# Performance work log

Measured on AMD Instinct MI355X. Metric: run time of the kernel, lower is better.

## Reference

```python
import jax, jax.numpy as jnp
import numpy as np

B, L, N, C = 64, 12, 4096, 3
FD, HD, OUT = 32, 64, 12
TID, DIW, TD = 288, 7, 16
STEPS = 4
EMB = 10  # node embedding dim for learned adjacency


def setup_inputs() -> dict:
    key = jax.random.key(0)
    ks = jax.random.split(key, 16)
    g = lambda i, shape, s=0.05: jax.random.normal(ks[i], shape, dtype=jnp.float32) * s
    z = lambda n: jnp.zeros((n,), jnp.float32)
    return {
        "history_data": jax.random.uniform(ks[0], (B, L, N, C), dtype=jnp.float32),
        "future_data": jnp.zeros((B, L, N, 1), jnp.float32),
        "batch_seen": 0,
        "epoch": 0,
        "train": 1,
        "tid_emb": g(1, (TID, TD)),
        "diw_emb": g(2, (DIW, TD)),
        "t2f_w": g(3, (2 * TD, FD)), "t2f_b": z(FD),
        "enc_w1": g(4, (L * C, HD)), "enc_b1": z(HD),
        "enc_w2": g(5, (HD, FD)), "enc_b2": z(FD),
        "node_emb": g(6, (N, EMB), 1.0),
        "pde_w1": g(7, (FD, HD)), "pde_b1": z(HD),
        "pde_w2": g(8, (HD, FD)), "pde_b2": z(FD),
        "ss_win": g(9, (FD, FD)), "ss_wst": g(10, (FD, FD)), "ss_b": z(FD),
        "ss_wout": g(11, (FD, FD)), "ss_bout": z(FD),
        "dec_w1": g(12, (FD, HD)), "dec_b1": z(HD),
        "dec_w2": g(13, (HD, OUT)), "dec_b2": z(OUT),
        "pde_mix": jnp.array(0.5, jnp.float32),
    }


def reference(history_data, future_data, batch_seen, epoch, train,
              tid_emb, diw_emb, t2f_w, t2f_b,
              enc_w1, enc_b1, enc_w2, enc_b2,
              node_emb,
              pde_w1, pde_b1, pde_w2, pde_b2,
              ss_win, ss_wst, ss_b, ss_wout, ss_bout,
              dec_w1, dec_b1, dec_w2, dec_b2, pde_mix):
    # --- encoder: per-node MLP over flattened (L, C) history ---
    x = history_data[..., :C]                                    # [B,L,N,C]
    x = jnp.transpose(x, (0, 2, 1, 3)).reshape(B, N, L * C)      # [B,N,L*C]
    field = jnp.maximum(x @ enc_w1 + enc_b1, 0.0) @ enc_w2 + enc_b2  # [B,N,FD]

    # --- temporal field bias from last-step tid/diw ---
    tid_idx = jnp.clip((history_data[:, -1, :, 1] * TID).astype(jnp.int32), 0, TID - 1)
    diw_idx = jnp.clip((history_data[:, -1, :, 2] * DIW).astype(jnp.int32), 0, DIW - 1)
    temp = jnp.concatenate([tid_emb[tid_idx], diw_emb[diw_idx]], axis=-1)  # [B,N,2*TD]
    field = field + temp @ t2f_w + t2f_b

    # --- learned adjacency for graph Laplacian (L = I - A) ---
    A = jax.nn.softmax(jnp.maximum(node_emb @ node_emb.T, 0.0), axis=-1)  # [N,N]

    alpha = jax.nn.sigmoid(pde_mix)
    dt = 1.0 / STEPS
    state = jnp.zeros_like(field)
    for _ in range(STEPS):  # fixed small unroll over PDE steps
        L_F = jnp.einsum('nm,bmf->bnf', A, field) - field         # (A - I) F
        N_F = jnp.maximum(field @ pde_w1 + pde_b1, 0.0) @ pde_w2 + pde_b2
        fe = field + (alpha * L_F + (1.0 - alpha) * N_F) * dt
        state = jnp.tanh(fe @ ss_win + state @ ss_wst + ss_b)     # state-space update
        field = fe + state @ ss_wout + ss_bout

    # --- decoder: per-node MLP to output horizon ---
    pred = jnp.maximum(field @ dec_w1 + dec_b1, 0.0) @ dec_w2 + dec_b2  # [B,N,OUT]
    return jnp.transpose(pred, (0, 2, 1))[..., None]              # [B,OUT,N,1]
```

## Files before the change

kernel.cpp:

```cpp
#include <hip/hip_runtime.h>

#define BATCH 64
#define LHIST 12
#define NNODE 4096
#define CCH   3
#define FD    32
#define HD    64
#define OUTD  12
#define TIDN  288
#define DIWN  7
#define TDD   16
#define EMBD  10
#define MROWS 2048
#define KDIM  4096
#define MTOT  (BATCH * NNODE)

typedef __attribute__((ext_vector_type(8))) short bf16x8;
typedef __attribute__((ext_vector_type(4))) float f32x4;

union BF8U { bf16x8 v; unsigned short s[8]; };

__device__ __forceinline__ unsigned short f2b(float f) {
    union { float f; unsigned u; } v; v.f = f;
    unsigned r = v.u + 0x7fffu + ((v.u >> 16) & 1u);
    return (unsigned short)(r >> 16);
}

__device__ __forceinline__ float b2f(unsigned short u) {
    union { unsigned u; float f; } v; v.u = (unsigned)u << 16; return v.f;
}

__device__ __forceinline__ float fast_tanh(float x) {
    x = fminf(fmaxf(x, -15.f), 15.f);
    const float e = __expf(2.f * x);
    return (e - 1.f) / (e + 1.f);
}

__device__ __forceinline__ void gl2lds16(const void* g, void* l) {
    __builtin_amdgcn_global_load_lds((__attribute__((address_space(1))) void*)(void*)g,
                                     (__attribute__((address_space(3))) void*)l, 16, 0, 0);
}

__device__ __forceinline__ bf16x8 ldsfrag(const unsigned short* p) {
    return *(const bf16x8*)p;
}

__device__ __forceinline__ bf16x8 pack8(float4 a, float4 b) {
    BF8U u;
    u.s[0] = f2b(a.x); u.s[1] = f2b(a.y); u.s[2] = f2b(a.z); u.s[3] = f2b(a.w);
    u.s[4] = f2b(b.x); u.s[5] = f2b(b.y); u.s[6] = f2b(b.z); u.s[7] = f2b(b.w);
    return u.v;
}

__global__ __launch_bounds__(256) void build_A(const float* __restrict__ emb,
                                               unsigned short* __restrict__ A) {
    const int n = blockIdx.x;
    const int tid = threadIdx.x;
    __shared__ float sc[NNODE];
    __shared__ float red[256];
    float e[EMBD];
#pragma unroll
    for (int c = 0; c < EMBD; c++) e[c] = emb[(size_t)n * EMBD + c];
    float mx = 0.f;
    for (int m = tid; m < NNODE; m += 256) {
        float s = 0.f;
#pragma unroll
        for (int c = 0; c < EMBD; c++) s += e[c] * emb[(size_t)m * EMBD + c];
        s = fmaxf(s, 0.f);
        sc[m] = s;
        mx = fmaxf(mx, s);
    }
    red[tid] = mx;
    __syncthreads();
    for (int off = 128; off > 0; off >>= 1) {
        if (tid < off) red[tid] = fmaxf(red[tid], red[tid + off]);
        __syncthreads();
    }
    mx = red[0];
    __syncthreads();
    float sum = 0.f;
    for (int m = tid; m < NNODE; m += 256) {
        float v = expf(sc[m] - mx);
        sc[m] = v;
        sum += v;
    }
    red[tid] = sum;
    __syncthreads();
    for (int off = 128; off > 0; off >>= 1) {
        if (tid < off) red[tid] += red[tid + off];
        __syncthreads();
    }
    const float inv = 1.f / red[0];
    for (int m = tid; m < NNODE; m += 256)
        A[(size_t)n * NNODE + m] = f2b(sc[m] * inv);
}

__global__ __launch_bounds__(256, 2) void encoder(const float* __restrict__ hist,
                                                  const float* __restrict__ tid_emb,
                                                  const float* __restrict__ diw_emb,
                                                  const float* __restrict__ t2f_w,
                                                  const float* __restrict__ t2f_b,
                                                  const float* __restrict__ enc_w1,
                                                  const float* __restrict__ enc_b1,
                                                  const float* __restrict__ enc_w2,
                                                  const float* __restrict__ enc_b2,
                                                  float* __restrict__ field,
                                                  unsigned short* __restrict__ fT) {
    const int gid = blockIdx.x * 256 + threadIdx.x;
    const int b = gid >> 12;
    const int n = gid & (NNODE - 1);
    const float* hb = hist + ((size_t)b * LHIST * NNODE + n) * CCH;
    float x[LHIST * CCH];
#pragma unroll
    for (int l = 0; l < LHIST; l++) {
        x[l * 3 + 0] = hb[(size_t)l * NNODE * CCH + 0];
        x[l * 3 + 1] = hb[(size_t)l * NNODE * CCH + 1];
        x[l * 3 + 2] = hb[(size_t)l * NNODE * CCH + 2];
    }
    float f[FD];
#pragma unroll
    for (int o = 0; o < FD; o++) f[o] = enc_b2[o] + t2f_b[o];
    for (int j = 0; j < HD; j++) {
        float h = enc_b1[j];
#pragma unroll
        for (int k = 0; k < LHIST * CCH; k++) h += x[k] * enc_w1[k * HD + j];
        h = fmaxf(h, 0.f);
#pragma unroll
        for (int o = 0; o < FD; o++) f[o] += h * enc_w2[j * FD + o];
    }
    const int ti = min(max((int)(x[11 * 3 + 1] * 288.0f), 0), TIDN - 1);
    const int di = min(max((int)(x[11 * 3 + 2] * 7.0f), 0), DIWN - 1);
    for (int g = 0; g < TDD; g++) {
        const float tg = tid_emb[ti * TDD + g];
        const float dg = diw_emb[di * TDD + g];
#pragma unroll
        for (int o = 0; o < FD; o++)
            f[o] += tg * t2f_w[g * FD + o] + dg * t2f_w[(TDD + g) * FD + o];
    }
#pragma unroll
    for (int o4 = 0; o4 < FD / 4; o4++) {
        float4 v = {f[o4 * 4 + 0], f[o4 * 4 + 1], f[o4 * 4 + 2], f[o4 * 4 + 3]};
        *(float4*)&field[(size_t)gid * FD + o4 * 4] = v;
    }
#pragma unroll
    for (int o = 0; o < FD; o++)
        fT[(size_t)(b * FD + o) * NNODE + n] = f2b(f[o]);
}

#define TPAD 36
#define QHP  72
#define QFP  40
__global__ __launch_bounds__(256) void gemm_step(const unsigned short* __restrict__ X,
                                                 const unsigned short* __restrict__ Y,
                                                 float* __restrict__ field,
                                                 unsigned short* __restrict__ state,
                                                 unsigned short* __restrict__ fTo,
                                                 const float* __restrict__ pde_w1,
                                                 const float* __restrict__ pde_b1,
                                                 const float* __restrict__ pde_w2,
                                                 const float* __restrict__ pde_b2,
                                                 const float* __restrict__ ss_win,
                                                 const float* __restrict__ ss_wst,
                                                 const float* __restrict__ ss_b,
                                                 const float* __restrict__ ss_wout,
                                                 const float* __restrict__ ss_bout,
                                                 const float* __restrict__ pde_mix,
                                                 int first) {
    constexpr int K = KDIM;
    constexpr int BK = 32;
    __shared__ __align__(16) unsigned short SM0[512 * TPAD];
    __shared__ __align__(16) unsigned short W1T[HD * FD];
    __shared__ __align__(16) unsigned short W2T[FD * HD];
    __shared__ __align__(16) unsigned short WinT[FD * FD];
    __shared__ __align__(16) unsigned short WstT[FD * FD];
    __shared__ __align__(16) unsigned short WoutT[FD * FD];
    __shared__ __align__(16) unsigned short Hs[4 * 32 * QHP];
    __shared__ __align__(16) unsigned short Fs[4 * 32 * QFP];

    const int tid = threadIdx.x;
    const int wave = tid >> 6;
    const int lane = tid & 63;

    for (int i = tid; i < HD * FD; i += 256) W1T[(i & 63) * FD + (i >> 6)] = f2b(pde_w1[i]);
    for (int i = tid; i < HD * FD; i += 256) W2T[(i & 31) * HD + (i >> 5)] = f2b(pde_w2[i]);
    for (int i = tid; i < FD * FD; i += 256) {
        WinT [(i & 31) * FD + (i >> 5)] = f2b(ss_win[i]);
        WstT [(i & 31) * FD + (i >> 5)] = f2b(ss_wst[i]);
        WoutT[(i & 31) * FD + (i >> 5)] = f2b(ss_wout[i]);
    }

    const int l = blockIdx.x + 16 * blockIdx.y;
    const int xcd = l & 7;
    const int rem = l >> 3;
    const int by = xcd * 4 + (rem & 3);
    const int bx = rem >> 2;
    const int i0 = bx * 128;
    const int j0 = by * 128;
    const int b0 = i0 >> 5;

    const int wi = (wave >> 1) * 64;
    const int wj = (wave & 1) * 64;

    const int lrow = lane >> 2;
    const int gcol = ((lane & 3) ^ ((lane >> 3) & 3)) * 8;

    const unsigned short* Xg = X + (size_t)(i0 + wave * 32 + lrow) * K + gcol;
    const unsigned short* Yg = Y + (size_t)(j0 + wave * 32 + lrow) * K + gcol;
    unsigned short* XsB = SM0;
    unsigned short* YsB = SM0 + 8192;
    unsigned short* Xd0 = XsB + (wave * 32) * BK;
    unsigned short* Xd1 = XsB + (wave * 32 + 16) * BK;
    unsigned short* Yd0 = YsB + (wave * 32) * BK;
    unsigned short* Yd1 = YsB + (wave * 32 + 16) * BK;

    const f32x4 zero = {0.f, 0.f, 0.f, 0.f};
    f32x4 acc[4][4];
#pragma unroll
    for (int a = 0; a < 4; a++)
#pragma unroll
        for (int b = 0; b < 4; b++) acc[a][b] = zero;

    const int fr = lane & 15;
    const int q = lane >> 4;
    const int kq8 = (q ^ ((fr >> 1) & 3)) * 8;

#define GS_ISSUE(P, KT)                                        \
    gl2lds16(Xg + (KT), Xd0 + (P) * 4096);                     \
    gl2lds16(Xg + (KT) + 16 * K, Xd1 + (P) * 4096);            \
    gl2lds16(Yg + (KT), Yd0 + (P) * 4096);                     \
    gl2lds16(Yg + (KT) + 16 * K, Yd1 + (P) * 4096);

#define GS_COMPUTE(P)                                                                 \
    {                                                                                 \
        bf16x8 fa[4], fb[4];                                                          \
        _Pragma("unroll") for (int t = 0; t < 4; t++)                                 \
            fa[t] = *(const bf16x8*)&XsB[(P) * 4096 + (wi + t * 16 + fr) * BK + kq8]; \
        _Pragma("unroll") for (int t = 0; t < 4; t++)                                 \
            fb[t] = *(const bf16x8*)&YsB[(P) * 4096 + (wj + t * 16 + fr) * BK + kq8]; \
        _Pragma("unroll") for (int mi = 0; mi < 4; mi++)                              \
            _Pragma("unroll") for (int ni = 0; ni < 4; ni++)                          \
                acc[mi][ni] = __builtin_amdgcn_mfma_f32_16x16x32_bf16(                \
                    fa[mi], fb[ni], acc[mi][ni], 0, 0, 0);                            \
    }

    GS_ISSUE(0, 0);
    __syncthreads();
    int p = 0;
    for (int kt = 0; kt < K; kt += BK) {
        if (kt + BK < K) { GS_ISSUE(p ^ 1, kt + BK); }
        GS_COMPUTE(p);
        __syncthreads();
        p ^= 1;
    }
#undef GS_COMPUTE
#undef GS_ISSUE

    unsigned short* T = SM0;
    const int r0 = q * 4;
#pragma unroll
    for (int mi = 0; mi < 4; mi++) {
#pragma unroll
        for (int ni = 0; ni < 4; ni++) {
            const int R0 = i0 + wi + mi * 16 + r0;
            const int nl = wj + ni * 16 + fr;
            ushort4 pk = {f2b(acc[mi][ni][0]), f2b(acc[mi][ni][1]),
                          f2b(acc[mi][ni][2]), f2b(acc[mi][ni][3])};
            *(ushort4*)&T[((((R0 >> 5) & 3) << 7) + nl) * TPAD + (R0 & 31)] = pk;
        }
    }
    __syncthreads();

    const int ln = fr;
    const int kq = q * 8;
    unsigned short* Hw = &Hs[wave * 32 * QHP];
    unsigned short* Fw = &Fs[wave * 32 * QFP];
    const float alpha = 1.f / (1.f + __expf(-pde_mix[0]));
    const float dt = 0.25f;

    bf16x8 w1f[4], w2f[2][2], winf[2], wstf[2], woutf[2];
#pragma unroll
    for (int nj = 0; nj < 4; nj++) w1f[nj] = ldsfrag(&W1T[(nj * 16 + ln) * FD + kq]);
#pragma unroll
    for (int nf = 0; nf < 2; nf++) {
#pragma unroll
        for (int kk = 0; kk < 2; kk++)
            w2f[nf][kk] = ldsfrag(&W2T[(nf * 16 + ln) * HD + kk * 32 + kq]);
        winf[nf]  = ldsfrag(&WinT [(nf * 16 + ln) * FD + kq]);
        wstf[nf]  = ldsfrag(&WstT [(nf * 16 + ln) * FD + kq]);
        woutf[nf] = ldsfrag(&WoutT[(nf * 16 + ln) * FD + kq]);
    }
    float b1v[4], b2v[2], bsv[2], bov[2];
#pragma unroll
    for (int nj = 0; nj < 4; nj++) b1v[nj] = pde_b1[nj * 16 + ln];
#pragma unroll
    for (int nf = 0; nf < 2; nf++) {
        b2v[nf] = pde_b2[nf * 16 + ln];
        bsv[nf] = ss_b[nf * 16 + ln];
        bov[nf] = ss_bout[nf * 16 + ln];
    }

    for (int qtr = 0; qtr < 4; qtr++) {
        const int lb = wave * 128 + qtr * 32;
        const int bb = lb >> 7;
        const int nl0 = lb & 127;
        const int bg = b0 + bb;
        const int mwg = (bg << 12) + j0 + nl0;

        bf16x8 fA[2], stA[2];
#pragma unroll
        for (int mi = 0; mi < 2; mi++) {
            const float4* fp = (const float4*)&field[(size_t)(mwg + mi * 16 + ln) * FD + kq];
            fA[mi] = pack8(fp[0], fp[1]);
        }
        if (!first) {
#pragma unroll
            for (int mi = 0; mi < 2; mi++)
                stA[mi] = *(const bf16x8*)&state[(size_t)(mwg + mi * 16 + ln) * FD + kq];
        }

        f32x4 hc[2][4];
#pragma unroll
        for (int mi = 0; mi < 2; mi++)
#pragma unroll
            for (int nj = 0; nj < 4; nj++)
                hc[mi][nj] = __builtin_amdgcn_mfma_f32_16x16x32_bf16(fA[mi], w1f[nj], zero, 0, 0, 0);
#pragma unroll
        for (int mi = 0; mi < 2; mi++)
#pragma unroll
            for (int nj = 0; nj < 4; nj++)
#pragma unroll
                for (int r = 0; r < 4; r++)
                    Hw[(mi * 16 + r0 + r) * QHP + nj * 16 + ln] =
                        f2b(fmaxf(hc[mi][nj][r] + b1v[nj], 0.f));

        float fld[2][2][4], ctv[2][2][4];
#pragma unroll
        for (int mi = 0; mi < 2; mi++)
#pragma unroll
            for (int nf = 0; nf < 2; nf++)
#pragma unroll
                for (int r = 0; r < 4; r++) {
                    const size_t idx = (size_t)(mwg + mi * 16 + r0 + r) * FD + nf * 16 + ln;
                    fld[mi][nf][r] = field[idx];
                    ctv[mi][nf][r] = b2f(T[(lb + mi * 16 + r0 + r) * TPAD + nf * 16 + ln]);
                }

        bf16x8 hA[2][2];
#pragma unroll
        for (int mi = 0; mi < 2; mi++)
#pragma unroll
            for (int kk = 0; kk < 2; kk++)
                hA[mi][kk] = ldsfrag(&Hw[(mi * 16 + ln) * QHP + kk * 32 + kq]);
        f32x4 nc[2][2];
#pragma unroll
        for (int mi = 0; mi < 2; mi++)
#pragma unroll
            for (int nf = 0; nf < 2; nf++) {
                f32x4 a = __builtin_amdgcn_mfma_f32_16x16x32_bf16(hA[mi][0], w2f[nf][0], zero, 0, 0, 0);
                nc[mi][nf] = __builtin_amdgcn_mfma_f32_16x16x32_bf16(hA[mi][1], w2f[nf][1], a, 0, 0, 0);
            }

        float fe[2][2][4];
#pragma unroll
        for (int mi = 0; mi < 2; mi++)
#pragma unroll
            for (int nf = 0; nf < 2; nf++)
#pragma unroll
                for (int r = 0; r < 4; r++) {
                    const float nfv = nc[mi][nf][r] + b2v[nf];
                    const float fv = fld[mi][nf][r];
                    fe[mi][nf][r] = fv + (alpha * (ctv[mi][nf][r] - fv) + (1.f - alpha) * nfv) * dt;
                    Fw[(mi * 16 + r0 + r) * QFP + nf * 16 + ln] = f2b(fe[mi][nf][r]);
                }

        bf16x8 feA[2];
#pragma unroll
        for (int mi = 0; mi < 2; mi++) feA[mi] = ldsfrag(&Fw[(mi * 16 + ln) * QFP + kq]);
        f32x4 sc_[2][2];
#pragma unroll
        for (int mi = 0; mi < 2; mi++)
#pragma unroll
            for (int nf = 0; nf < 2; nf++) {
                f32x4 a = __builtin_amdgcn_mfma_f32_16x16x32_bf16(feA[mi], winf[nf], zero, 0, 0, 0);
                if (!first)
                    a = __builtin_amdgcn_mfma_f32_16x16x32_bf16(stA[mi], wstf[nf], a, 0, 0, 0);
                sc_[mi][nf] = a;
            }
        float sval[2][2][4];
#pragma unroll
        for (int mi = 0; mi < 2; mi++)
#pragma unroll
            for (int nf = 0; nf < 2; nf++)
#pragma unroll
                for (int r = 0; r < 4; r++)
                    sval[mi][nf][r] = fast_tanh(sc_[mi][nf][r] + bsv[nf]);
#pragma unroll
        for (int mi = 0; mi < 2; mi++)
#pragma unroll
            for (int nf = 0; nf < 2; nf++)
#pragma unroll
                for (int r = 0; r < 4; r++)
                    Fw[(mi * 16 + r0 + r) * QFP + nf * 16 + ln] = f2b(sval[mi][nf][r]);

        bf16x8 SA[2];
#pragma unroll
        for (int mi = 0; mi < 2; mi++) SA[mi] = ldsfrag(&Fw[(mi * 16 + ln) * QFP + kq]);
#pragma unroll
        for (int mi = 0; mi < 2; mi++) {
#pragma unroll
            for (int nf = 0; nf < 2; nf++) {
                f32x4 oc = __builtin_amdgcn_mfma_f32_16x16x32_bf16(SA[mi], woutf[nf], zero, 0, 0, 0);
                float fnew[4];
#pragma unroll
                for (int r = 0; r < 4; r++) {
                    fnew[r] = fe[mi][nf][r] + oc[r] + bov[nf];
                    const size_t idx = (size_t)(mwg + mi * 16 + r0 + r) * FD + nf * 16 + ln;
                    field[idx] = fnew[r];
                    state[idx] = f2b(sval[mi][nf][r]);
                }
                ushort4 pk = {f2b(fnew[0]), f2b(fnew[1]), f2b(fnew[2]), f2b(fnew[3])};
                const size_t fta = (size_t)(bg * FD + nf * 16 + ln) * NNODE
                                 + j0 + nl0 + mi * 16 + r0;
                *(ushort4*)&fTo[fta] = pk;
            }
        }
    }
}

__global__ __launch_bounds__(256) void gemm_bt(const unsigned short* __restrict__ X,
                                               const unsigned short* __restrict__ Y,
                                               unsigned short* __restrict__ Cp) {
    constexpr int K = KDIM;
    constexpr int KS = KDIM / 2;
    constexpr int BK = 32;
    __shared__ __align__(16) unsigned short Xs[2 * 4096];
    __shared__ __align__(16) unsigned short Ys[2 * 4096];
    const int tid = threadIdx.x;
    const int wave = tid >> 6;
    const int lane = tid & 63;

    const int l = blockIdx.x + 16 * blockIdx.y;
    const int xcd = l & 7;
    const int rem = l >> 3;
    const int by = xcd * 4 + (rem & 3);
    const int bx = rem >> 2;
    const int i0 = bx * 128;
    const int j0 = by * 128;
    const int k0 = blockIdx.z * KS;
    unsigned short* C = Cp + (size_t)blockIdx.z * MTOT * FD;

    const int wi = (wave >> 1) * 64;
    const int wj = (wave & 1) * 64;

    const int lrow = lane >> 2;
    const int gcol = ((lane & 3) ^ ((lane >> 3) & 3)) * 8;

    const unsigned short* Xg = X + (size_t)(i0 + wave * 32 + lrow) * K + k0 + gcol;
    const unsigned short* Yg = Y + (size_t)(j0 + wave * 32 + lrow) * K + k0 + gcol;
    unsigned short* Xd0 = Xs + (wave * 32) * BK;
    unsigned short* Xd1 = Xs + (wave * 32 + 16) * BK;
    unsigned short* Yd0 = Ys + (wave * 32) * BK;
    unsigned short* Yd1 = Ys + (wave * 32 + 16) * BK;

    const f32x4 zero = {0.f, 0.f, 0.f, 0.f};
    f32x4 acc[4][4];
#pragma unroll
    for (int a = 0; a < 4; a++)
#pragma unroll
        for (int b = 0; b < 4; b++) acc[a][b] = zero;

    const int fr = lane & 15;
    const int q = lane >> 4;
    const int kq8 = (q ^ ((fr >> 1) & 3)) * 8;

#define GB_ISSUE(P, KT)                                        \
    gl2lds16(Xg + (KT), Xd0 + (P) * 4096);                     \
    gl2lds16(Xg + (KT) + 16 * K, Xd1 + (P) * 4096);            \
    gl2lds16(Yg + (KT), Yd0 + (P) * 4096);                     \
    gl2lds16(Yg + (KT) + 16 * K, Yd1 + (P) * 4096);

#define GB_COMPUTE(P)                                                                \
    {                                                                                \
        bf16x8 fa[4], fb[4];                                                         \
        _Pragma("unroll") for (int t = 0; t < 4; t++)                                \
            fa[t] = *(const bf16x8*)&Xs[(P) * 4096 + (wi + t * 16 + fr) * BK + kq8]; \
        _Pragma("unroll") for (int t = 0; t < 4; t++)                                \
            fb[t] = *(const bf16x8*)&Ys[(P) * 4096 + (wj + t * 16 + fr) * BK + kq8]; \
        _Pragma("unroll") for (int mi = 0; mi < 4; mi++)                             \
            _Pragma("unroll") for (int ni = 0; ni < 4; ni++)                         \
                acc[mi][ni] = __builtin_amdgcn_mfma_f32_16x16x32_bf16(               \
                    fa[mi], fb[ni], acc[mi][ni], 0, 0, 0);                           \
    }

    GB_ISSUE(0, 0);
    __syncthreads();
    int p = 0;
    for (int kt = 0; kt < KS; kt += BK) {
        if (kt + BK < KS) { GB_ISSUE(p ^ 1, kt + BK); }
        GB_COMPUTE(p);
        __syncthreads();
        p ^= 1;
    }
#undef GB_COMPUTE
#undef GB_ISSUE

    const int r0 = q * 4;
#pragma unroll
    for (int mi = 0; mi < 4; mi++) {
#pragma unroll
        for (int ni = 0; ni < 4; ni++) {
            const int R0 = i0 + wi + mi * 16 + r0;
            const int col = j0 + wj + ni * 16 + fr;
            const size_t addr = ((size_t)(R0 >> 5) * NNODE + col) * FD + (R0 & 31);
            ushort4 pk = {f2b(acc[mi][ni][0]), f2b(acc[mi][ni][1]),
                          f2b(acc[mi][ni][2]), f2b(acc[mi][ni][3])};
            *(ushort4*)&C[addr] = pk;
        }
    }
}

#define HPAD 72
#define FPAD 40
__global__ __launch_bounds__(256, 2) void step_mfma(const unsigned short* __restrict__ Ct0,
                                                    const unsigned short* __restrict__ Ct1,
                                                    float* __restrict__ field,
                                                    unsigned short* __restrict__ state,
                                                    const float* __restrict__ pde_w1,
                                                    const float* __restrict__ pde_b1,
                                                    const float* __restrict__ pde_w2,
                                                    const float* __restrict__ pde_b2,
                                                    const float* __restrict__ ss_win,
                                                    const float* __restrict__ ss_wst,
                                                    const float* __restrict__ ss_b,
                                                    const float* __restrict__ ss_wout,
                                                    const float* __restrict__ ss_bout,
                                                    const float* __restrict__ pde_mix,
                                                    const float* __restrict__ dec_w1,
                                                    const float* __restrict__ dec_b1,
                                                    const float* __restrict__ dec_w2,
                                                    const float* __restrict__ dec_b2,
                                                    float* __restrict__ out) {
    __shared__ __align__(16) unsigned short W1T[HD * FD];
    __shared__ __align__(16) unsigned short W2T[FD * HD];
    __shared__ __align__(16) unsigned short WinT[FD * FD];
    __shared__ __align__(16) unsigned short WstT[FD * FD];
    __shared__ __align__(16) unsigned short WoutT[FD * FD];
    __shared__ __align__(16) unsigned short Wd1T[HD * FD];
    __shared__ __align__(16) unsigned short Wd2T[16 * HD];
    __shared__ __align__(16) unsigned short Hs[4 * 64 * HPAD];
    __shared__ __align__(16) unsigned short Fs[4 * 64 * FPAD];

    const int tid = threadIdx.x;
    for (int i = tid; i < HD * FD; i += 256) W1T[(i & 63) * FD + (i >> 6)] = f2b(pde_w1[i]);
    for (int i = tid; i < HD * FD; i += 256) W2T[(i & 31) * HD + (i >> 5)] = f2b(pde_w2[i]);
    for (int i = tid; i < FD * FD; i += 256) {
        WinT [(i & 31) * FD + (i >> 5)] = f2b(ss_win[i]);
        WstT [(i & 31) * FD + (i >> 5)] = f2b(ss_wst[i]);
        WoutT[(i & 31) * FD + (i >> 5)] = f2b(ss_wout[i]);
    }
    for (int i = tid; i < HD * FD; i += 256)
        Wd1T[(i & 63) * FD + (i >> 6)] = f2b(dec_w1[i]);
    for (int i = tid; i < 16 * HD; i += 256) {
        const int o = i >> 6, j = i & 63;
        Wd2T[i] = (o < OUTD) ? f2b(dec_w2[j * OUTD + o]) : (unsigned short)0;
    }
    __syncthreads();

    const int wv = tid >> 6;
    const int lane = tid & 63;
    const int ln = lane & 15;
    const int q = lane >> 4;
    const int kq = q * 8;
    const int r0 = q * 4;
    const int mw = blockIdx.x * 256 + wv * 64;
    const int b = mw >> 12;
    const int n0 = mw & (NNODE - 1);
    unsigned short* Hw = &Hs[wv * 64 * HPAD];
    unsigned short* Fw = &Fs[wv * 64 * FPAD];

    const float alpha = 1.f / (1.f + __expf(-pde_mix[0]));
    const float dt = 0.25f;

    bf16x8 w1f[4], w2f[2][2], winf[2], wstf[2], woutf[2];
#pragma unroll
    for (int nj = 0; nj < 4; nj++) w1f[nj] = ldsfrag(&W1T[(nj * 16 + ln) * FD + kq]);
#pragma unroll
    for (int nf = 0; nf < 2; nf++) {
#pragma unroll
        for (int kk = 0; kk < 2; kk++)
            w2f[nf][kk] = ldsfrag(&W2T[(nf * 16 + ln) * HD + kk * 32 + kq]);
        winf[nf]  = ldsfrag(&WinT [(nf * 16 + ln) * FD + kq]);
        wstf[nf]  = ldsfrag(&WstT [(nf * 16 + ln) * FD + kq]);
        woutf[nf] = ldsfrag(&WoutT[(nf * 16 + ln) * FD + kq]);
    }

    float b1v[4], b2v[2], bsv[2], bov[2];
#pragma unroll
    for (int nj = 0; nj < 4; nj++) b1v[nj] = pde_b1[nj * 16 + ln];
#pragma unroll
    for (int nf = 0; nf < 2; nf++) {
        b2v[nf] = pde_b2[nf * 16 + ln];
        bsv[nf] = ss_b[nf * 16 + ln];
        bov[nf] = ss_bout[nf * 16 + ln];
    }

    bf16x8 fA[4], stA[4];
#pragma unroll
    for (int mi = 0; mi < 4; mi++) {
        const float4* fp = (const float4*)&field[(size_t)(mw + mi * 16 + ln) * FD + kq];
        fA[mi] = pack8(fp[0], fp[1]);
    }
#pragma unroll
    for (int mi = 0; mi < 4; mi++)
        stA[mi] = *(const bf16x8*)&state[(size_t)(mw + mi * 16 + ln) * FD + kq];

    const f32x4 zero = {0.f, 0.f, 0.f, 0.f};

    f32x4 hc[4][4];
#pragma unroll
    for (int mi = 0; mi < 4; mi++)
#pragma unroll
        for (int nj = 0; nj < 4; nj++)
            hc[mi][nj] = __builtin_amdgcn_mfma_f32_16x16x32_bf16(fA[mi], w1f[nj], zero, 0, 0, 0);
#pragma unroll
    for (int mi = 0; mi < 4; mi++)
#pragma unroll
        for (int nj = 0; nj < 4; nj++)
#pragma unroll
            for (int r = 0; r < 4; r++)
                Hw[(mi * 16 + r0 + r) * HPAD + nj * 16 + ln] =
                    f2b(fmaxf(hc[mi][nj][r] + b1v[nj], 0.f));

    float fld[4][2][4], ctv[4][2][4];
#pragma unroll
    for (int mi = 0; mi < 4; mi++)
#pragma unroll
        for (int nf = 0; nf < 2; nf++)
#pragma unroll
            for (int r = 0; r < 4; r++) {
                const size_t idx = (size_t)(mw + mi * 16 + r0 + r) * FD + nf * 16 + ln;
                fld[mi][nf][r] = field[idx];
                ctv[mi][nf][r] = b2f(Ct0[idx]) + b2f(Ct1[idx]);
            }

    bf16x8 hA[4][2];
#pragma unroll
    for (int mi = 0; mi < 4; mi++)
#pragma unroll
        for (int kk = 0; kk < 2; kk++)
            hA[mi][kk] = ldsfrag(&Hw[(mi * 16 + ln) * HPAD + kk * 32 + kq]);
    f32x4 nc[4][2];
#pragma unroll
    for (int mi = 0; mi < 4; mi++)
#pragma unroll
        for (int nf = 0; nf < 2; nf++) {
            f32x4 a = __builtin_amdgcn_mfma_f32_16x16x32_bf16(hA[mi][0], w2f[nf][0], zero, 0, 0, 0);
            nc[mi][nf] = __builtin_amdgcn_mfma_f32_16x16x32_bf16(hA[mi][1], w2f[nf][1], a, 0, 0, 0);
        }

    float fe[4][2][4];
#pragma unroll
    for (int mi = 0; mi < 4; mi++)
#pragma unroll
        for (int nf = 0; nf < 2; nf++)
#pragma unroll
            for (int r = 0; r < 4; r++) {
                const float nfv = nc[mi][nf][r] + b2v[nf];
                const float fv = fld[mi][nf][r];
                fe[mi][nf][r] = fv + (alpha * (ctv[mi][nf][r] - fv) + (1.f - alpha) * nfv) * dt;
                Fw[(mi * 16 + r0 + r) * FPAD + nf * 16 + ln] = f2b(fe[mi][nf][r]);
            }

    bf16x8 feA[4];
#pragma unroll
    for (int mi = 0; mi < 4; mi++) feA[mi] = ldsfrag(&Fw[(mi * 16 + ln) * FPAD + kq]);
    f32x4 sc_[4][2];
#pragma unroll
    for (int mi = 0; mi < 4; mi++)
#pragma unroll
        for (int nf = 0; nf < 2; nf++) {
            f32x4 a = __builtin_amdgcn_mfma_f32_16x16x32_bf16(feA[mi], winf[nf], zero, 0, 0, 0);
            a = __builtin_amdgcn_mfma_f32_16x16x32_bf16(stA[mi], wstf[nf], a, 0, 0, 0);
            sc_[mi][nf] = a;
        }
    float sval[4][2][4];
#pragma unroll
    for (int mi = 0; mi < 4; mi++)
#pragma unroll
        for (int nf = 0; nf < 2; nf++)
#pragma unroll
            for (int r = 0; r < 4; r++)
                sval[mi][nf][r] = fast_tanh(sc_[mi][nf][r] + bsv[nf]);
#pragma unroll
    for (int mi = 0; mi < 4; mi++)
#pragma unroll
        for (int nf = 0; nf < 2; nf++)
#pragma unroll
            for (int r = 0; r < 4; r++)
                Fw[(mi * 16 + r0 + r) * FPAD + nf * 16 + ln] = f2b(sval[mi][nf][r]);

    bf16x8 SA[4];
#pragma unroll
    for (int mi = 0; mi < 4; mi++) SA[mi] = ldsfrag(&Fw[(mi * 16 + ln) * FPAD + kq]);
    float fnew[4][2][4];
#pragma unroll
    for (int mi = 0; mi < 4; mi++)
#pragma unroll
        for (int nf = 0; nf < 2; nf++) {
            f32x4 oc = __builtin_amdgcn_mfma_f32_16x16x32_bf16(SA[mi], woutf[nf], zero, 0, 0, 0);
#pragma unroll
            for (int r = 0; r < 4; r++)
                fnew[mi][nf][r] = fe[mi][nf][r] + oc[r] + bov[nf];
        }

    bf16x8 wd1f[4], wd2f[2];
#pragma unroll
    for (int nj = 0; nj < 4; nj++) wd1f[nj] = ldsfrag(&Wd1T[(nj * 16 + ln) * FD + kq]);
#pragma unroll
    for (int kk = 0; kk < 2; kk++) wd2f[kk] = ldsfrag(&Wd2T[ln * HD + kk * 32 + kq]);
    float db1v[4];
#pragma unroll
    for (int nj = 0; nj < 4; nj++) db1v[nj] = dec_b1[nj * 16 + ln];
    const float db2v = (ln < OUTD) ? dec_b2[ln] : 0.f;

#pragma unroll
    for (int mi = 0; mi < 4; mi++)
#pragma unroll
        for (int nf = 0; nf < 2; nf++)
#pragma unroll
            for (int r = 0; r < 4; r++)
                Fw[(mi * 16 + r0 + r) * FPAD + nf * 16 + ln] = f2b(fnew[mi][nf][r]);
    bf16x8 fnA[4];
#pragma unroll
    for (int mi = 0; mi < 4; mi++) fnA[mi] = ldsfrag(&Fw[(mi * 16 + ln) * FPAD + kq]);

    f32x4 h2[4][4];
#pragma unroll
    for (int mi = 0; mi < 4; mi++)
#pragma unroll
        for (int nj = 0; nj < 4; nj++)
            h2[mi][nj] = __builtin_amdgcn_mfma_f32_16x16x32_bf16(fnA[mi], wd1f[nj], zero, 0, 0, 0);
#pragma unroll
    for (int mi = 0; mi < 4; mi++)
#pragma unroll
        for (int nj = 0; nj < 4; nj++)
#pragma unroll
            for (int r = 0; r < 4; r++)
                Hw[(mi * 16 + r0 + r) * HPAD + nj * 16 + ln] =
                    f2b(fmaxf(h2[mi][nj][r] + db1v[nj], 0.f));
    bf16x8 h2A[4][2];
#pragma unroll
    for (int mi = 0; mi < 4; mi++)
#pragma unroll
        for (int kk = 0; kk < 2; kk++)
            h2A[mi][kk] = ldsfrag(&Hw[(mi * 16 + ln) * HPAD + kk * 32 + kq]);
#pragma unroll
    for (int mi = 0; mi < 4; mi++) {
        f32x4 a = __builtin_amdgcn_mfma_f32_16x16x32_bf16(h2A[mi][0], wd2f[0], zero, 0, 0, 0);
        a = __builtin_amdgcn_mfma_f32_16x16x32_bf16(h2A[mi][1], wd2f[1], a, 0, 0, 0);
        if (ln < OUTD) {
            float4 v = {a[0] + db2v, a[1] + db2v, a[2] + db2v, a[3] + db2v};
            *(float4*)&out[(size_t)(b * OUTD + ln) * NNODE + n0 + mi * 16 + r0] = v;
        }
    }
}

extern "C" void kernel_launch(void* const* d_in, const int* in_sizes, int n_in,
                              void* d_out, int out_size, void* d_ws, size_t ws_size,
                              hipStream_t stream) {
    (void)in_sizes; (void)n_in; (void)out_size; (void)ws_size;
    const float* hist    = (const float*)d_in[0];
    const float* tid_emb = (const float*)d_in[5];
    const float* diw_emb = (const float*)d_in[6];
    const float* t2f_w   = (const float*)d_in[7];
    const float* t2f_b   = (const float*)d_in[8];
    const float* enc_w1  = (const float*)d_in[9];
    const float* enc_b1  = (const float*)d_in[10];
    const float* enc_w2  = (const float*)d_in[11];
    const float* enc_b2  = (const float*)d_in[12];
    const float* node_emb= (const float*)d_in[13];
    const float* pde_w1  = (const float*)d_in[14];
    const float* pde_b1  = (const float*)d_in[15];
    const float* pde_w2  = (const float*)d_in[16];
    const float* pde_b2  = (const float*)d_in[17];
    const float* ss_win  = (const float*)d_in[18];
    const float* ss_wst  = (const float*)d_in[19];
    const float* ss_b    = (const float*)d_in[20];
    const float* ss_wout = (const float*)d_in[21];
    const float* ss_bout = (const float*)d_in[22];
    const float* dec_w1  = (const float*)d_in[23];
    const float* dec_b1  = (const float*)d_in[24];
    const float* dec_w2  = (const float*)d_in[25];
    const float* dec_b2  = (const float*)d_in[26];
    const float* pde_mix = (const float*)d_in[27];

    char* w = (char*)d_ws;
    unsigned short* A_bf = (unsigned short*)w;  w += (size_t)KDIM * KDIM * 2;
    unsigned short* fTa  = (unsigned short*)w;  w += (size_t)MROWS * KDIM * 2;
    unsigned short* fTb  = (unsigned short*)w;  w += (size_t)MROWS * KDIM * 2;
    float* field = (float*)w;                   w += (size_t)MTOT * FD * 4;
    unsigned short* state = (unsigned short*)w; w += (size_t)MTOT * FD * 2;
    unsigned short* Cp    = (unsigned short*)w; w += (size_t)2 * MTOT * FD * 2;

    build_A<<<NNODE, 256, 0, stream>>>(node_emb, A_bf);
    encoder<<<(BATCH * NNODE) / 256, 256, 0, stream>>>(hist, tid_emb, diw_emb, t2f_w,
                                                       t2f_b, enc_w1, enc_b1, enc_w2,
                                                       enc_b2, field, fTa);
    unsigned short* fts[4] = {fTa, fTb, fTa, fTb};
    for (int s = 0; s < 3; s++) {
        gemm_step<<<dim3(16, 32), 256, 0, stream>>>(
            fts[s], A_bf, field, state, fts[s + 1], pde_w1, pde_b1, pde_w2, pde_b2,
            ss_win, ss_wst, ss_b, ss_wout, ss_bout, pde_mix, s == 0 ? 1 : 0);
    }
    gemm_bt<<<dim3(16, 32, 2), 256, 0, stream>>>(fts[3], A_bf, Cp);
    step_mfma<<<MTOT / 256, 256, 0, stream>>>(
        Cp, Cp + (size_t)MTOT * FD, field, state, pde_w1, pde_b1, pde_w2, pde_b2,
        ss_win, ss_wst, ss_b, ss_wout, ss_bout, pde_mix,
        dec_w1, dec_b1, dec_w2, dec_b2, (float*)d_out);
}
```

Before: 700.6 us.

## Merge adjacency build and encoder into one launch; register-staged gemm_bt prefetch

Fuses the build_A softmax kernel and the encoder into a single init kernel whose blocks branch on blockIdx, so the two independent phases can run concurrently and one launch is saved. In gemm_bt, the direct global-to-LDS async loads are replaced by register-staged loads with two tiles in flight, and the XOR swizzle is applied on the LDS store side. This is meant to hide global latency better across k-steps. In exchange it costs more registers, and the fused kernel carries encoder register pressure together with the build_A shared memory footprint.

Result: faster. 681.2 us (-2.8%).

```diff
diff --git a/kernel.cpp b/kernel.cpp
--- a/kernel.cpp
+++ b/kernel.cpp
@@ -52,99 +52,100 @@
     return u.v;
 }
 
-__global__ __launch_bounds__(256) void build_A(const float* __restrict__ emb,
-                                               unsigned short* __restrict__ A) {
-    const int n = blockIdx.x;
-    const int tid = threadIdx.x;
+__global__ __launch_bounds__(256, 2) void init_k(const float* __restrict__ emb,
+                                                 unsigned short* __restrict__ A,
+                                                 const float* __restrict__ hist,
+                                                 const float* __restrict__ tid_emb,
+                                                 const float* __restrict__ diw_emb,
+                                                 const float* __restrict__ t2f_w,
+                                                 const float* __restrict__ t2f_b,
+                                                 const float* __restrict__ enc_w1,
+                                                 const float* __restrict__ enc_b1,
+                                                 const float* __restrict__ enc_w2,
+                                                 const float* __restrict__ enc_b2,
+                                                 float* __restrict__ field,
+                                                 unsigned short* __restrict__ fT) {
     __shared__ float sc[NNODE];
     __shared__ float red[256];
-    float e[EMBD];
-#pragma unroll
-    for (int c = 0; c < EMBD; c++) e[c] = emb[(size_t)n * EMBD + c];
-    float mx = 0.f;
-    for (int m = tid; m < NNODE; m += 256) {
-        float s = 0.f;
-#pragma unroll
-        for (int c = 0; c < EMBD; c++) s += e[c] * emb[(size_t)m * EMBD + c];
-        s = fmaxf(s, 0.f);
-        sc[m] = s;
-        mx = fmaxf(mx, s);
-    }
-    red[tid] = mx;
-    __syncthreads();
-    for (int off = 128; off > 0; off >>= 1) {
-        if (tid < off) red[tid] = fmaxf(red[tid], red[tid + off]);
+    const int tid = threadIdx.x;
+    if (blockIdx.x < NNODE) {
+        const int n = blockIdx.x;
+        float e[EMBD];
+#pragma unroll
+        for (int c = 0; c < EMBD; c++) e[c] = emb[(size_t)n * EMBD + c];
+        float mx = 0.f;
+        for (int m = tid; m < NNODE; m += 256) {
+            float s = 0.f;
+#pragma unroll
+            for (int c = 0; c < EMBD; c++) s += e[c] * emb[(size_t)m * EMBD + c];
+            s = fmaxf(s, 0.f);
+            sc[m] = s;
+            mx = fmaxf(mx, s);
+        }
+        red[tid] = mx;
         __syncthreads();
-    }
-    mx = red[0];
-    __syncthreads();
-    float sum = 0.f;
-    for (int m = tid; m < NNODE; m += 256) {
-        float v = expf(sc[m] - mx);
-        sc[m] = v;
-        sum += v;
-    }
-    red[tid] = sum;
-    __syncthreads();
-    for (int off = 128; off > 0; off >>= 1) {
-        if (tid < off) red[tid] += red[tid + off];
+        for (int off = 128; off > 0; off >>= 1) {
+            if (tid < off) red[tid] = fmaxf(red[tid], red[tid + off]);
+            __syncthreads();
+        }
+        mx = red[0];
         __syncthreads();
-    }
-    const float inv = 1.f / red[0];
-    for (int m = tid; m < NNODE; m += 256)
-        A[(size_t)n * NNODE + m] = f2b(sc[m] * inv);
-}
-
-__global__ __launch_bounds__(256, 2) void encoder(const float* __restrict__ hist,
-                                                  const float* __restrict__ tid_emb,
-                                                  const float* __restrict__ diw_emb,
-                                                  const float* __restrict__ t2f_w,
-                                                  const float* __restrict__ t2f_b,
-                                                  const float* __restrict__ enc_w1,
-                                                  const float* __restrict__ enc_b1,
-                                                  const float* __restrict__ enc_w2,
-                                                  const float* __restrict__ enc_b2,
-                                                  float* __restrict__ field,
-                                                  unsigned short* __restrict__ fT) {
-    const int gid = blockIdx.x * 256 + threadIdx.x;
-    const int b = gid >> 12;
-    const int n = gid & (NNODE - 1);
-    const float* hb = hist + ((size_t)b * LHIST * NNODE + n) * CCH;
-    float x[LHIST * CCH];
-#pragma unroll
-    for (int l = 0; l < LHIST; l++) {
-        x[l * 3 + 0] = hb[(size_t)l * NNODE * CCH + 0];
-        x[l * 3 + 1] = hb[(size_t)l * NNODE * CCH + 1];
-        x[l * 3 + 2] = hb[(size_t)l * NNODE * CCH + 2];
-    }
-    float f[FD];
-#pragma unroll
-    for (int o = 0; o < FD; o++) f[o] = enc_b2[o] + t2f_b[o];
-    for (int j = 0; j < HD; j++) {
-        float h = enc_b1[j];
-#pragma unroll
-        for (int k = 0; k < LHIST * CCH; k++) h += x[k] * enc_w1[k * HD + j];
-        h = fmaxf(h, 0.f);
-#pragma unroll
-        for (int o = 0; o < FD; o++) f[o] += h * enc_w2[j * FD + o];
-    }
-    const int ti = min(max((int)(x[11 * 3 + 1] * 288.0f), 0), TIDN - 1);
-    const int di = min(max((int)(x[11 * 3 + 2] * 7.0f), 0), DIWN - 1);
-    for (int g = 0; g < TDD; g++) {
-        const float tg = tid_emb[ti * TDD + g];
-        const float dg = diw_emb[di * TDD + g];
+        float sum = 0.f;
+        for (int m = tid; m < NNODE; m += 256) {
+            float v = expf(sc[m] - mx);
+            sc[m] = v;
+            sum += v;
+        }
+        red[tid] = sum;
+        __syncthreads();
+        for (int off = 128; off > 0; off >>= 1) {
+            if (tid < off) red[tid] += red[tid + off];
+            __syncthreads();
+        }
+        const float inv = 1.f / red[0];
+        for (int m = tid; m < NNODE; m += 256)
+            A[(size_t)n * NNODE + m] = f2b(sc[m] * inv);
+    } else {
+        const int gid = (blockIdx.x - NNODE) * 256 + tid;
+        const int b = gid >> 12;
+        const int n = gid & (NNODE - 1);
+        const float* hb = hist + ((size_t)b * LHIST * NNODE + n) * CCH;
+        float x[LHIST * CCH];
+#pragma unroll
+        for (int l = 0; l < LHIST; l++) {
+            x[l * 3 + 0] = hb[(size_t)l * NNODE * CCH + 0];
+            x[l * 3 + 1] = hb[(size_t)l * NNODE * CCH + 1];
+            x[l * 3 + 2] = hb[(size_t)l * NNODE * CCH + 2];
+        }
+        float f[FD];
+#pragma unroll
+        for (int o = 0; o < FD; o++) f[o] = enc_b2[o] + t2f_b[o];
+        for (int j = 0; j < HD; j++) {
+            float h = enc_b1[j];
+#pragma unroll
+            for (int k = 0; k < LHIST * CCH; k++) h += x[k] * enc_w1[k * HD + j];
+            h = fmaxf(h, 0.f);
+#pragma unroll
+            for (int o = 0; o < FD; o++) f[o] += h * enc_w2[j * FD + o];
+        }
+        const int ti = min(max((int)(x[11 * 3 + 1] * 288.0f), 0), TIDN - 1);
+        const int di = min(max((int)(x[11 * 3 + 2] * 7.0f), 0), DIWN - 1);
+        for (int g = 0; g < TDD; g++) {
+            const float tg = tid_emb[ti * TDD + g];
+            const float dg = diw_emb[di * TDD + g];
+#pragma unroll
+            for (int o = 0; o < FD; o++)
+                f[o] += tg * t2f_w[g * FD + o] + dg * t2f_w[(TDD + g) * FD + o];
+        }
+#pragma unroll
+        for (int o4 = 0; o4 < FD / 4; o4++) {
+            float4 v = {f[o4 * 4 + 0], f[o4 * 4 + 1], f[o4 * 4 + 2], f[o4 * 4 + 3]};
+            *(float4*)&field[(size_t)gid * FD + o4 * 4] = v;
+        }
 #pragma unroll
         for (int o = 0; o < FD; o++)
-            f[o] += tg * t2f_w[g * FD + o] + dg * t2f_w[(TDD + g) * FD + o];
-    }
-#pragma unroll
-    for (int o4 = 0; o4 < FD / 4; o4++) {
-        float4 v = {f[o4 * 4 + 0], f[o4 * 4 + 1], f[o4 * 4 + 2], f[o4 * 4 + 3]};
-        *(float4*)&field[(size_t)gid * FD + o4 * 4] = v;
-    }
-#pragma unroll
-    for (int o = 0; o < FD; o++)
-        fT[(size_t)(b * FD + o) * NNODE + n] = f2b(f[o]);
+            fT[(size_t)(b * FD + o) * NNODE + n] = f2b(f[o]);
+    }
 }
 
 #define TPAD 36
@@ -453,14 +454,13 @@
     const int wj = (wave & 1) * 64;
 
     const int lrow = lane >> 2;
-    const int gcol = ((lane & 3) ^ ((lane >> 3) & 3)) * 8;
+    const int gcol = (lane & 3) * 8;
+    const int scol = ((lane & 3) ^ ((lane >> 3) & 3)) * 8;
 
     const unsigned short* Xg = X + (size_t)(i0 + wave * 32 + lrow) * K + k0 + gcol;
     const unsigned short* Yg = Y + (size_t)(j0 + wave * 32 + lrow) * K + k0 + gcol;
-    unsigned short* Xd0 = Xs + (wave * 32) * BK;
-    unsigned short* Xd1 = Xs + (wave * 32 + 16) * BK;
-    unsigned short* Yd0 = Ys + (wave * 32) * BK;
-    unsigned short* Yd1 = Ys + (wave * 32 + 16) * BK;
+    const int ld0 = (wave * 32 + lrow) * BK + scol;
+    const int ld1 = (wave * 32 + 16 + lrow) * BK + scol;
 
     const f32x4 zero = {0.f, 0.f, 0.f, 0.f};
     f32x4 acc[4][4];
@@ -473,36 +473,60 @@
     const int q = lane >> 4;
     const int kq8 = (q ^ ((fr >> 1) & 3)) * 8;
 
-#define GB_ISSUE(P, KT)                                        \
-    gl2lds16(Xg + (KT), Xd0 + (P) * 4096);                     \
-    gl2lds16(Xg + (KT) + 16 * K, Xd1 + (P) * 4096);            \
-    gl2lds16(Yg + (KT), Yd0 + (P) * 4096);                     \
-    gl2lds16(Yg + (KT) + 16 * K, Yd1 + (P) * 4096);
-
-#define GB_COMPUTE(P)                                                                \
-    {                                                                                \
-        bf16x8 fa[4], fb[4];                                                         \
-        _Pragma("unroll") for (int t = 0; t < 4; t++)                                \
+#define GB_COMPUTE(P)                                                              \
+    {                                                                              \
+        bf16x8 fa[4], fb[4];                                                       \
+        _Pragma("unroll") for (int t = 0; t < 4; t++)                              \
             fa[t] = *(const bf16x8*)&Xs[(P) * 4096 + (wi + t * 16 + fr) * BK + kq8]; \
-        _Pragma("unroll") for (int t = 0; t < 4; t++)                                \
+        _Pragma("unroll") for (int t = 0; t < 4; t++)                              \
             fb[t] = *(const bf16x8*)&Ys[(P) * 4096 + (wj + t * 16 + fr) * BK + kq8]; \
-        _Pragma("unroll") for (int mi = 0; mi < 4; mi++)                             \
-            _Pragma("unroll") for (int ni = 0; ni < 4; ni++)                         \
-                acc[mi][ni] = __builtin_amdgcn_mfma_f32_16x16x32_bf16(               \
-                    fa[mi], fb[ni], acc[mi][ni], 0, 0, 0);                           \
-    }
-
-    GB_ISSUE(0, 0);
+        _Pragma("unroll") for (int mi = 0; mi < 4; mi++)                           \
+            _Pragma("unroll") for (int ni = 0; ni < 4; ni++)                       \
+                acc[mi][ni] = __builtin_amdgcn_mfma_f32_16x16x32_bf16(             \
+                    fa[mi], fb[ni], acc[mi][ni], 0, 0, 0);                         \
+    }
+
+    uint4 ax0 = *(const uint4*)(Xg);
+    uint4 ax1 = *(const uint4*)(Xg + 16 * K);
+    uint4 ay0 = *(const uint4*)(Yg);
+    uint4 ay1 = *(const uint4*)(Yg + 16 * K);
+    uint4 bx0 = *(const uint4*)(Xg + BK);
+    uint4 bx1 = *(const uint4*)(Xg + BK + 16 * K);
+    uint4 by0 = *(const uint4*)(Yg + BK);
+    uint4 by1 = *(const uint4*)(Yg + BK + 16 * K);
+    *(uint4*)&Xs[ld0] = ax0; *(uint4*)&Xs[ld1] = ax1;
+    *(uint4*)&Ys[ld0] = ay0; *(uint4*)&Ys[ld1] = ay1;
     __syncthreads();
+
     int p = 0;
-    for (int kt = 0; kt < KS; kt += BK) {
-        if (kt + BK < KS) { GB_ISSUE(p ^ 1, kt + BK); }
+    for (int kt = 0; kt < KS; kt += 2 * BK) {
+        if (kt + 2 * BK < KS) {
+            ax0 = *(const uint4*)(Xg + kt + 2 * BK);
+            ax1 = *(const uint4*)(Xg + kt + 2 * BK + 16 * K);
+            ay0 = *(const uint4*)(Yg + kt + 2 * BK);
+            ay1 = *(const uint4*)(Yg + kt + 2 * BK + 16 * K);
+        }
         GB_COMPUTE(p);
-        __syncthreads();
-        p ^= 1;
+        {
+            const int np = p ^ 1;
+            *(uint4*)&Xs[np * 4096 + ld0] = bx0; *(uint4*)&Xs[np * 4096 + ld1] = bx1;
+            *(uint4*)&Ys[np * 4096 + ld0] = by0; *(uint4*)&Ys[np * 4096 + ld1] = by1;
+            __syncthreads();
+        }
+        if (kt + 3 * BK < KS) {
+            bx0 = *(const uint4*)(Xg + kt + 3 * BK);
+            bx1 = *(const uint4*)(Xg + kt + 3 * BK + 16 * K);
+            by0 = *(const uint4*)(Yg + kt + 3 * BK);
+            by1 = *(const uint4*)(Yg + kt + 3 * BK + 16 * K);
+        }
+        GB_COMPUTE(p ^ 1);
+        if (kt + 2 * BK < KS) {
+            *(uint4*)&Xs[p * 4096 + ld0] = ax0; *(uint4*)&Xs[p * 4096 + ld1] = ax1;
+            *(uint4*)&Ys[p * 4096 + ld0] = ay0; *(uint4*)&Ys[p * 4096 + ld1] = ay1;
+            __syncthreads();
+        }
     }
 #undef GB_COMPUTE
-#undef GB_ISSUE
 
     const int r0 = q * 4;
 #pragma unroll
@@ -802,10 +826,9 @@
     unsigned short* state = (unsigned short*)w; w += (size_t)MTOT * FD * 2;
     unsigned short* Cp    = (unsigned short*)w; w += (size_t)2 * MTOT * FD * 2;
 
-    build_A<<<NNODE, 256, 0, stream>>>(node_emb, A_bf);
-    encoder<<<(BATCH * NNODE) / 256, 256, 0, stream>>>(hist, tid_emb, diw_emb, t2f_w,
-                                                       t2f_b, enc_w1, enc_b1, enc_w2,
-                                                       enc_b2, field, fTa);
+    init_k<<<NNODE + MTOT / 256, 256, 0, stream>>>(node_emb, A_bf, hist, tid_emb,
+                                                   diw_emb, t2f_w, t2f_b, enc_w1,
+                                                   enc_b1, enc_w2, enc_b2, field, fTa);
     unsigned short* fts[4] = {fTa, fTb, fTa, fTb};
     for (int s = 0; s < 3; s++) {
         gemm_step<<<dim3(16, 32), 256, 0, stream>>>(
```
